# Optimization experiments

Measured on AMD Instinct MI355X. Metric: run time of the kernel, lower is better.

The kernel has to match this reference:

```python
import jax, jax.numpy as jnp
import numpy as np

B, S, T, H, E, V = 32, 400, 32, 512, 128, 50000
A = H  # attention feature dim

def setup_inputs() -> dict:
    key = jax.random.key(0)
    ks = jax.random.split(key, 16)
    f = lambda k, shape: jax.random.normal(k, shape, dtype=jnp.float32) * 0.02
    return {
        "source_tokens": jax.random.randint(ks[0], (B, S), 0, V, dtype=jnp.int32),
        "embedded_tgt": jax.random.normal(ks[1], (B, T, E), dtype=jnp.float32),
        "encoder_states": jax.random.normal(ks[2], (B, S, 2 * H), dtype=jnp.float32),
        "source_mask": jnp.ones((B, S), dtype=bool),
        "h0": f(ks[3], (B, H)),
        "c0": f(ks[4], (B, H)),
        "W_ih": f(ks[5], (4 * H, E)),
        "W_hh": f(ks[6], (4 * H, H)),
        "b_ih": jnp.zeros((4 * H,), jnp.float32),
        "b_hh": jnp.zeros((4 * H,), jnp.float32),
        "W_enc": f(ks[7], (2 * H, A)),
        "W_dec": f(ks[8], (H, A)),
        "w_cov": f(ks[9], (A,)),
        "b_att": jnp.zeros((A,), jnp.float32),
        "v_att": f(ks[10], (A,)),
        "W_ah": f(ks[11], (3 * H, H)),
        "b_ah": jnp.zeros((H,), jnp.float32),
        "W_pg": f(ks[12], (3 * H + E, 1)),
        "b_pg": jnp.zeros((1,), jnp.float32),
        "W_v": f(ks[13], (H, V)),
        "b_v": jnp.zeros((V,), jnp.float32),
    }


def reference(source_tokens, embedded_tgt, encoder_states, source_mask, h0, c0,
              W_ih, W_hh, b_ih, b_hh, W_enc, W_dec, w_cov, b_att, v_att,
              W_ah, b_ah, W_pg, b_pg, W_v, b_v):
    Bn, Sn = source_tokens.shape
    # precompute encoder projection for Bahdanau attention: (B,S,A)
    enc_proj = jnp.einsum('bsd,da->bsa', encoder_states, W_enc)
    bidx = jnp.arange(Bn)[:, None]
    NEG = jnp.float32(-1e9)
    EPS = jnp.float32(1e-20)

    def step(carry, emb):  # emb: (B,E)
        h, c, cov = carry
        # LSTM cell (torch gate order i,f,g,o)
        gates = emb @ W_ih.T + h @ W_hh.T + b_ih + b_hh
        i, fg, g, o = jnp.split(gates, 4, axis=-1)
        c = jax.nn.sigmoid(fg) * c + jax.nn.sigmoid(i) * jnp.tanh(g)
        h = jax.nn.sigmoid(o) * jnp.tanh(c)
        # coverage attention
        feat = jnp.tanh(enc_proj + (h @ W_dec)[:, None, :] + cov[:, :, None] * w_cov + b_att)
        scores = jnp.where(source_mask, feat @ v_att, NEG)  # (B,S)
        attn = jax.nn.softmax(scores, axis=-1)
        context = jnp.einsum('bs,bsd->bd', attn, encoder_states)  # (B,2H)
        cov = cov + attn
        ah = jnp.tanh(jnp.concatenate([context, h], axis=-1) @ W_ah + b_ah)  # (B,H)
        p_gen = jax.nn.sigmoid(jnp.concatenate([context, h, emb], axis=-1) @ W_pg + b_pg)  # (B,1)
        vocab_dist = p_gen * jax.nn.softmax(ah @ W_v + b_v, axis=-1)  # (B,V)
        attn_dist = (1.0 - p_gen) * attn  # (B,S)
        final = vocab_dist.at[bidx, source_tokens].add(attn_dist)  # copy-merge scatter_add
        logp = jnp.log(final + EPS)
        return (h, c, cov), (logp, ah, attn, cov, p_gen[:, 0])

    cov0 = jnp.zeros_like(source_mask, dtype=jnp.float32)
    _, (logps, dec_states, attns, covs, p_gens) = jax.lax.scan(
        step, (h0, c0, cov0), jnp.swapaxes(embedded_tgt, 0, 1))
    tr = lambda x: jnp.swapaxes(x, 0, 1)  # (T,B,...) -> (B,T,...)
    return tr(logps), tr(dec_states), tr(attns), tr(covs), tr(p_gens)
```

## Files before the change

### kernel.cpp

```cpp
#include <hip/hip_runtime.h>
#include <hip/hip_bf16.h>
#include <stdint.h>
#include <stddef.h>

#define B_  32
#define S_  400
#define T_  32
#define H_  512
#define E_  128
#define V_  50000
#define A_  512
#define H2_ 1024
#define H3_ 1536
#define H4_ 2048
#define R_  1024
#define PGK_ 1664
#define NBLKV_ 391
#define GRB_ 128
#define WROW_ 520

typedef unsigned short u16;
typedef short v8s __attribute__((ext_vector_type(8)));
typedef float v4f __attribute__((ext_vector_type(4)));

__device__ __forceinline__ float fsig(float x){ return 1.0f/(1.0f + __expf(-x)); }
__device__ __forceinline__ float ftanh(float x){ float e = __expf(2.0f*x); return 1.0f - 2.0f/(e + 1.0f); }
__device__ __forceinline__ u16 f2bf(float x){ __hip_bfloat16 b = __float2bfloat16(x); return *reinterpret_cast<u16*>(&b); }
__device__ __forceinline__ float bf2f(u16 u){ __hip_bfloat16 b = *reinterpret_cast<__hip_bfloat16*>(&u); return __bfloat162float(b); }

__device__ __forceinline__ float wsum(float v){
  #pragma unroll
  for (int off = 32; off > 0; off >>= 1) v += __shfl_xor(v, off, 64);
  return v;
}
__device__ __forceinline__ float wmax(float v){
  #pragma unroll
  for (int off = 32; off > 0; off >>= 1) v = fmaxf(v, __shfl_xor(v, off, 64));
  return v;
}

#define ALD(p)    __hip_atomic_load((p), __ATOMIC_RELAXED, __HIP_MEMORY_SCOPE_AGENT)
#define AST(p,v)  __hip_atomic_store((p), (v), __ATOMIC_RELAXED, __HIP_MEMORY_SCOPE_AGENT)

__device__ __forceinline__ void ldsbar(){
  asm volatile("s_waitcnt lgkmcnt(0)" ::: "memory");
  __builtin_amdgcn_s_barrier();
  asm volatile("" ::: "memory");
}

__device__ __forceinline__ void gridbar2(unsigned* bar, unsigned target, int grp){
  __syncthreads();
  if (threadIdx.x == 0){
    unsigned v = __hip_atomic_fetch_add(bar + grp*32, 1u, __ATOMIC_RELAXED, __HIP_MEMORY_SCOPE_AGENT);
    if (v == target*16u - 1u){
      unsigned g2 = __hip_atomic_fetch_add(bar + 256, 1u, __ATOMIC_RELAXED, __HIP_MEMORY_SCOPE_AGENT);
      if (g2 == target*8u - 1u)
        AST(bar + 288, target);
    }
    while (ALD(bar + 288) < target) __builtin_amdgcn_s_sleep(2);
    asm volatile("" ::: "memory");
  }
  __syncthreads();
}


__global__ void k_init0(unsigned* __restrict__ bar, unsigned long long* __restrict__ mz){
  int t = threadIdx.x;
  if (t < 512) AST(bar + t, 0u);
  if (t < 256) AST(mz + t, 0ull);
}

__global__ __launch_bounds__(256) void k_transpose(const float* __restrict__ in, float* __restrict__ out, int R, int C){
  __shared__ float tile[64][65];
  int c0 = blockIdx.x*64, r0 = blockIdx.y*64;
  int tid = threadIdx.x;
  int cl = tid & 63, q = tid >> 6;
  #pragma unroll
  for (int i=0;i<16;i++){
    int r = q + i*4;
    float v = 0.0f;
    if (r0 + r < R && c0 + cl < C) v = in[(size_t)(r0+r)*C + c0 + cl];
    tile[r][cl] = v;
  }
  __syncthreads();
  #pragma unroll
  for (int i=0;i<16;i++){
    int c = q + i*4;
    if (c0 + c < C && r0 + cl < R)
      out[(size_t)(c0+c)*R + r0 + cl] = tile[cl][c];
  }
}

__global__ __launch_bounds__(256) void k_convT(const float* __restrict__ in, u16* __restrict__ hi, int R, int C){
  __shared__ float tile[64][65];
  int c0 = blockIdx.x*64, r0 = blockIdx.y*64;
  int tid = threadIdx.x;
  int cl = tid & 63, q = tid >> 6;
  #pragma unroll
  for (int i=0;i<16;i++){
    int r = q + i*4;
    float v = 0.0f;
    if (r0 + r < R && c0 + cl < C) v = in[(size_t)(r0+r)*C + c0 + cl];
    tile[r][cl] = v;
  }
  __syncthreads();
  #pragma unroll
  for (int i=0;i<16;i++){
    int c = q + i*4;
    if (c0 + c < C && r0 + cl < R)
      hi[(size_t)(c0+c)*R + r0 + cl] = f2bf(tile[cl][c]);
  }
}

__global__ __launch_bounds__(256) void k_convT3(const float* __restrict__ in, u16* __restrict__ out){
  __shared__ float tile[64][65];
  int c0 = blockIdx.x*64, r0 = blockIdx.y*64;
  int tid = threadIdx.x;
  int cl = tid & 63, q = tid >> 6;
  #pragma unroll
  for (int i=0;i<16;i++){
    int r = q + i*4;
    tile[r][cl] = in[(size_t)(r0+r)*A_ + c0 + cl];
  }
  __syncthreads();
  #pragma unroll
  for (int i=0;i<16;i++){
    int c = q + i*4;
    float v = tile[cl][c];
    u16 h = f2bf(v);
    u16 lo = f2bf(v - bf2f(h));
    size_t o = (size_t)(c0+c)*3072 + (r0+cl);
    out[o] = h;
    out[o + 1024] = lo;
    out[o + 2048] = h;
  }
}

__global__ void k_conv3(const float* __restrict__ in, u16* __restrict__ out, int n4){
  int i = blockIdx.x*256 + threadIdx.x;
  if (i >= n4) return;
  float4 x = reinterpret_cast<const float4*>(in)[i];
  u16 h0v=f2bf(x.x), h1v=f2bf(x.y), h2v=f2bf(x.z), h3v=f2bf(x.w);
  uint2 hv; hv.x = (unsigned)h0v | ((unsigned)h1v << 16); hv.y = (unsigned)h2v | ((unsigned)h3v << 16);
  uint2 lv;
  lv.x = (unsigned)f2bf(x.x - bf2f(h0v)) | ((unsigned)f2bf(x.y - bf2f(h1v)) << 16);
  lv.y = (unsigned)f2bf(x.z - bf2f(h2v)) | ((unsigned)f2bf(x.w - bf2f(h3v)) << 16);
  int row = i >> 8, c = (i & 255)*4;
  size_t base = (size_t)row*3072 + c;
  *reinterpret_cast<uint2*>(out + base)        = hv;
  *reinterpret_cast<uint2*>(out + base + 1024) = hv;
  *reinterpret_cast<uint2*>(out + base + 2048) = lv;
}

__global__ __launch_bounds__(256) void k_gih(const float* __restrict__ emb, const float* __restrict__ WihT,
    const float* __restrict__ b_ih, const float* __restrict__ b_hh, float* __restrict__ G){
  __shared__ float em[8][128];
  int r0 = blockIdx.x*8;
  int tid = threadIdx.x;
  #pragma unroll
  for (int i=0;i<4;i++){
    int e = i*256 + tid;
    em[e>>7][e&127] = emb[(size_t)(r0 + (e>>7))*E_ + (e&127)];
  }
  __syncthreads();
  for (int jj=0;jj<8;jj++){
    int j = jj*256 + tid;
    float bias = b_ih[j] + b_hh[j];
    float acc[8];
    #pragma unroll
    for (int r=0;r<8;r++) acc[r] = bias;
    for (int e=0;e<128;e++){
      float wv = WihT[(size_t)e*H4_ + j];
      #pragma unroll
      for (int r=0;r<8;r++) acc[r] += em[r][e]*wv;
    }
    #pragma unroll
    for (int rr=0;rr<8;rr++){
      int r = r0 + rr;
      G[(size_t)(r & 31)*65536 + (size_t)(j >> 9)*16384 + (size_t)(j & 511)*32 + (r >> 5)] = acc[rr];
    }
  }
}

__global__ __launch_bounds__(256, 2) void k_gemm_bf16(
    const u16* __restrict__ A, int lda, const u16* __restrict__ Bt, int ldb,
    const float* __restrict__ bias, float* __restrict__ Cf, u16* __restrict__ Cbf, int ldc,
    int M, int N, int K, float2* __restrict__ stats, int nblk)
{
  __shared__ __align__(16) float CsF[128*132];
  __shared__ float rs[128], rs2[128];
  u16* As = reinterpret_cast<u16*>(CsF);
  u16* Bs = As + 128*64;
  const int tid = threadIdx.x;
  const int m0 = blockIdx.y * 128;
  const int n0 = blockIdx.x * 128;
  const int l  = tid & 63;
  const int wavebase = tid & ~63;
  const int wid = tid >> 6;
  const int wm = (wid >> 1) * 64;
  const int wn = (wid & 1) * 64;

  v4f acc[4][4];
  v4f vzero = {0.0f, 0.0f, 0.0f, 0.0f};
  #pragma unroll
  for (int i=0;i<4;i++)
    #pragma unroll
    for (int j=0;j<4;j++) acc[i][j] = vzero;

  for (int k0 = 0; k0 < K; k0 += 64){
    __syncthreads();
    #pragma unroll
    for (int jj=0;jj<4;jj++){
      int fc = jj*256 + tid;
      int row = fc >> 3;
      int cc = (fc & 7) ^ (row & 7);
      const u16* g = A + (size_t)(m0 + row)*lda + k0 + cc*8;
      __builtin_amdgcn_global_load_lds(
        (__attribute__((address_space(1))) void*)g,
        (__attribute__((address_space(3))) void*)(As + (size_t)(jj*256 + wavebase)*8),
        16, 0, 0);
    }
    #pragma unroll
    for (int jj=0;jj<4;jj++){
      int fc = jj*256 + tid;
      int row = fc >> 3;
      int cc = (fc & 7) ^ (row & 7);
      int rn = n0 + row; if (rn > N-1) rn = N-1;
      const u16* g = Bt + (size_t)rn*ldb + k0 + cc*8;
      __builtin_amdgcn_global_load_lds(
        (__attribute__((address_space(1))) void*)g,
        (__attribute__((address_space(3))) void*)(Bs + (size_t)(jj*256 + wavebase)*8),
        16, 0, 0);
    }
    __syncthreads();
    #pragma unroll
    for (int ks=0;ks<2;ks++){
      v8s af[4], bfr[4];
      #pragma unroll
      for (int rt=0;rt<4;rt++){
        int r = wm + rt*16 + (l & 15);
        int cs = (ks*4 + (l >> 4)) ^ (r & 7);
        af[rt] = *reinterpret_cast<const v8s*>(As + r*64 + cs*8);
      }
      #pragma unroll
      for (int nt=0;nt<4;nt++){
        int r = wn + nt*16 + (l & 15);
        int cs = (ks*4 + (l >> 4)) ^ (r & 7);
        bfr[nt] = *reinterpret_cast<const v8s*>(Bs + r*64 + cs*8);
      }
      #pragma unroll
      for (int rt=0;rt<4;rt++)
        #pragma unroll
        for (int nt=0;nt<4;nt++)
          acc[rt][nt] = __builtin_amdgcn_mfma_f32_16x16x32_bf16(af[rt], bfr[nt], acc[rt][nt], 0, 0, 0);
    }
  }

  const int cl = l & 15;
  const int rg = (l >> 4) * 4;
  float cvv[4][4][4];
  #pragma unroll
  for (int rt=0;rt<4;rt++)
    #pragma unroll
    for (int nt=0;nt<4;nt++){
      int gc = n0 + wn + nt*16 + cl;
      float bv = (bias && gc < N) ? bias[gc] : 0.0f;
      #pragma unroll
      for (int i=0;i<4;i++) cvv[rt][nt][i] = acc[rt][nt][i] + bv;
    }

  if (stats){
    float tsm[4][4];
    #pragma unroll
    for (int rt=0;rt<4;rt++)
      #pragma unroll
      for (int i=0;i<4;i++){
        float mx = -1e30f;
        #pragma unroll
        for (int nt=0;nt<4;nt++){
          int gc = n0 + wn + nt*16 + cl;
          if (gc < N) mx = fmaxf(mx, cvv[rt][nt][i]);
        }
        #pragma unroll
        for (int off=1; off<16; off<<=1) mx = fmaxf(mx, __shfl_xor(mx, off, 64));
        if (wn == 0 && cl == 0) rs[wm + rt*16 + rg + i] = mx;
        tsm[rt][i] = mx;
      }
    __syncthreads();
    if (wn != 0){
      #pragma unroll
      for (int rt=0;rt<4;rt++)
        #pragma unroll
        for (int i=0;i<4;i++){
          float c = fmaxf(tsm[rt][i], rs[wm + rt*16 + rg + i]);
          if (cl == 0) rs[wm + rt*16 + rg + i] = c;
        }
    }
    __syncthreads();
    #pragma unroll
    for (int rt=0;rt<4;rt++)
      #pragma unroll
      for (int i=0;i<4;i++){
        float rm = rs[wm + rt*16 + rg + i];
        float sm = 0.0f;
        #pragma unroll
        for (int nt=0;nt<4;nt++){
          int gc = n0 + wn + nt*16 + cl;
          if (gc < N) sm += __expf(cvv[rt][nt][i] - rm);
        }
        #pragma unroll
        for (int off=1; off<16; off<<=1) sm += __shfl_xor(sm, off, 64);
        tsm[rt][i] = sm;
        if (wn == 0 && cl == 0) rs2[wm + rt*16 + rg + i] = sm;
      }
    __syncthreads();
    if (wn != 0 && cl == 0){
      #pragma unroll
      for (int rt=0;rt<4;rt++)
        #pragma unroll
        for (int i=0;i<4;i++){
          int row = wm + rt*16 + rg + i;
          stats[(size_t)(m0 + row)*nblk + blockIdx.x] =
            make_float2(rs[row], tsm[rt][i] + rs2[row]);
        }
    }
  }

  __syncthreads();
  #pragma unroll
  for (int rt=0;rt<4;rt++)
    #pragma unroll
    for (int nt=0;nt<4;nt++)
      #pragma unroll
      for (int i=0;i<4;i++)
        CsF[(wm + rt*16 + rg + i)*132 + wn + nt*16 + cl] = cvv[rt][nt][i];
  __syncthreads();
  #pragma unroll
  for (int it=0; it<16; ++it){
    int row = (tid >> 5) + it*8;
    int c4 = tid & 31;
    int gc = n0 + c4*4;
    int gr = m0 + row;
    if (gc < N){
      float4 v = *reinterpret_cast<const float4*>(&CsF[row*132 + c4*4]);
      if (Cf) *reinterpret_cast<float4*>(Cf + (size_t)gr*ldc + gc) = v;
      if (Cbf){
        uint2 o;
        o.x = (unsigned)f2bf(v.x) | ((unsigned)f2bf(v.y) << 16);
        o.y = (unsigned)f2bf(v.z) | ((unsigned)f2bf(v.w) << 16);
        *reinterpret_cast<uint2*>(Cbf + (size_t)gr*ldc + gc) = o;
      }
    }
  }
}

__global__ __launch_bounds__(256) void k_wv_f32(
  const float* __restrict__ Aah, const float* __restrict__ Wv, const float* __restrict__ bv,
  float* __restrict__ Cl)
{
  __shared__ float Asf[32][68];
  __shared__ float Bsf[32][64];
  int n0 = blockIdx.x*64, m0 = blockIdx.y*64;
  int tid = threadIdx.x;
  int tx = tid & 15, ty = tid >> 4;
  float acc[4][4] = {};
  for (int kc = 0; kc < H_; kc += 32){
    __syncthreads();
    #pragma unroll
    for (int i=0;i<8;i++){
      int e = i*256 + tid;
      Asf[e & 31][e >> 5] = Aah[(size_t)(m0 + (e >> 5))*H_ + kc + (e & 31)];
    }
    #pragma unroll
    for (int i=0;i<8;i++){
      int e = i*256 + tid;
      int nc = n0 + (e & 63); if (nc >= V_) nc = V_-1;
      Bsf[e >> 6][e & 63] = Wv[(size_t)(kc + (e >> 6))*V_ + nc];
    }
    __syncthreads();
    #pragma unroll
    for (int k=0;k<32;k++){
      float4 a4 = *reinterpret_cast<const float4*>(&Asf[k][ty*4]);
      float4 b4 = *reinterpret_cast<const float4*>(&Bsf[k][tx*4]);
      float av[4] = {a4.x, a4.y, a4.z, a4.w};
      float bv4[4] = {b4.x, b4.y, b4.z, b4.w};
      #pragma unroll
      for (int i=0;i<4;i++)
        #pragma unroll
        for (int j=0;j<4;j++)
          acc[i][j] = __builtin_fmaf(av[i], bv4[j], acc[i][j]);
    }
  }
  #pragma unroll
  for (int i=0;i<4;i++){
    int rr = m0 + ty*4 + i;
    #pragma unroll
    for (int j=0;j<4;j++){
      int cc = n0 + tx*4 + j;
      if (cc < V_) Cl[(size_t)rr*V_ + cc] = acc[i][j] + bv[cc];
    }
  }
}

__global__ __launch_bounds__(1024) void k_recur(
  const float* __restrict__ W_hh, const float* __restrict__ G2,
  const float* __restrict__ W_decT, const u16* __restrict__ ep_bf,
  const float* __restrict__ w_cov, const float* __restrict__ v_att,
  const void* __restrict__ maskp, const float* __restrict__ h0,
  const float* __restrict__ c0, float* __restrict__ h_gT,
  float* __restrict__ dec_g, unsigned long long* __restrict__ mz,
  float* __restrict__ catbuf, float* __restrict__ attns, float* __restrict__ covs,
  unsigned* __restrict__ bar)
{
  const int beta = blockIdx.x;
  const int tid = threadIdx.x;
  __shared__ __align__(16) u16 Whi[32*WROW_];
  __shared__ __align__(16) u16 Wlo[32*WROW_];
  __shared__ __align__(16) u16 Hhi[32*WROW_];
  __shared__ __align__(16) u16 Hlo[32*WROW_];
  __shared__ float gv2[16][32];
  __shared__ float c_l[128];
  __shared__ float dec_l[512];
  __shared__ float sc_l[100];
  __shared__ float cov_l[100];
  __shared__ float smz[4][2];

  const int b32 = tid & 31;
  const int w = tid >> 6, l = tid & 63;
  const int grp = beta & 7;
  const int bb = (beta & 7)*4 + (beta >> 5);
  const int sq = (beta >> 3) & 3;
  const int b2 = (tid & 15)*2;
  const int kg = tid >> 4;

  for (int idx = tid; idx < 32*512; idx += 1024){
    int row = idx >> 9;
    int k = idx & 511;
    float v = 0.0f;
    if (row < 16)      v = W_hh[((size_t)(row >> 2)*H_ + beta*4 + (row & 3))*H_ + k];
    else if (row < 20) v = W_decT[(size_t)(beta*4 + (row - 16))*H_ + k];
    u16 h = f2bf(v);
    Whi[row*WROW_ + k] = h;
    Wlo[row*WROW_ + k] = f2bf(v - bf2f(h));
  }
  if (tid < 128) c_l[tid] = c0[(size_t)(tid & 31)*H_ + beta*4 + (tid >> 5)];
  if (tid < 100) cov_l[tid] = 0.f;

  const unsigned* m32p = (const unsigned*)maskp;
  const unsigned char* m8p = (const unsigned char*)maskp;
  const bool bytemode = (m32p[0] == 0x01010101u);

  float wc8[8], va8[8];
  {
    int a0 = l*8;
    #pragma unroll
    for (int j=0;j<8;j++){ wc8[j] = w_cov[a0+j]; va8[j] = v_att[a0+j]; }
  }

  float hA[8], hB[8];
  unsigned long long hld[8];
  #pragma unroll
  for (int kk=0;kk<8;kk++){
    int k = kg*8 + kk;
    hA[kk] = h0[(size_t)b2*H_ + k];
    hB[kk] = h0[(size_t)(b2+1)*H_ + k];
  }

  unsigned gen = 0;
  for (int i = 0; i <= T_ + 1; ++i){
    const int par = i & 1;
    {
      v8s phA, plA, phB, plB;
      #pragma unroll
      for (int kk=0;kk<8;kk++){
        float va = hA[kk], vb = hB[kk];
        u16 ha = f2bf(va), hb = f2bf(vb);
        phA[kk] = (short)ha; plA[kk] = (short)f2bf(va - bf2f(ha));
        phB[kk] = (short)hb; plB[kk] = (short)f2bf(vb - bf2f(hb));
      }
      *reinterpret_cast<v8s*>(Hhi + (size_t)b2*WROW_ + kg*8) = phA;
      *reinterpret_cast<v8s*>(Hlo + (size_t)b2*WROW_ + kg*8) = plA;
      *reinterpret_cast<v8s*>(Hhi + (size_t)(b2+1)*WROW_ + kg*8) = phB;
      *reinterpret_cast<v8s*>(Hlo + (size_t)(b2+1)*WROW_ + kg*8) = plB;
    }
    ldsbar();

    if (w < 4){
      const int mt = w >> 1, nt = w & 1;
      const int fr = (l & 15);
      const int fo = (l >> 4)*8;
      const u16* Ahi = Whi + (size_t)(mt*16 + fr)*WROW_ + fo;
      const u16* Alo = Wlo + (size_t)(mt*16 + fr)*WROW_ + fo;
      const u16* Bhi = Hhi + (size_t)(nt*16 + fr)*WROW_ + fo;
      const u16* Blo = Hlo + (size_t)(nt*16 + fr)*WROW_ + fo;
      v4f a0 = {0.f,0.f,0.f,0.f}, a1 = a0, a2 = a0;
      #pragma unroll
      for (int ks=0; ks<16; ks++){
        v8s wh = *reinterpret_cast<const v8s*>(Ahi + ks*32);
        v8s wl = *reinterpret_cast<const v8s*>(Alo + ks*32);
        v8s hh = *reinterpret_cast<const v8s*>(Bhi + ks*32);
        v8s hl = *reinterpret_cast<const v8s*>(Blo + ks*32);
        a0 = __builtin_amdgcn_mfma_f32_16x16x32_bf16(wh, hh, a0, 0, 0, 0);
        a1 = __builtin_amdgcn_mfma_f32_16x16x32_bf16(wh, hl, a1, 0, 0, 0);
        a2 = __builtin_amdgcn_mfma_f32_16x16x32_bf16(wl, hh, a2, 0, 0, 0);
      }
      v4f acc = a0 + a1 + a2;
      if (mt == 0){
        int col = nt*16 + fr;
        int r0w = (l >> 4)*4;
        #pragma unroll
        for (int q=0;q<4;q++) gv2[r0w + q][col] = acc[q];
      } else if ((l >> 4) == 0){
        int b = nt*16 + fr;
        float* dg = dec_g + (size_t)par*B_*A_ + (size_t)b*A_ + beta*4;
        unsigned long long p0 = ((unsigned long long)__float_as_uint(acc[1]) << 32) | __float_as_uint(acc[0]);
        unsigned long long p1 = ((unsigned long long)__float_as_uint(acc[3]) << 32) | __float_as_uint(acc[2]);
        AST(reinterpret_cast<unsigned long long*>(dg), p0);
        AST(reinterpret_cast<unsigned long long*>(dg + 2), p1);
      }
    }
    ldsbar();

    if (i < T_ && tid < 128){
      int hh = tid >> 5;
      int hidx = beta*4 + hh;
      const float* Gr = G2 + (size_t)i*65536 + (size_t)hidx*32 + b32;
      float gi = gv2[0*4+hh][b32] + Gr[0];
      float gf = gv2[1*4+hh][b32] + Gr[16384];
      float gz = gv2[2*4+hh][b32] + Gr[32768];
      float go = gv2[3*4+hh][b32] + Gr[49152];
      float co = c_l[tid];
      float cn = fsig(gf)*co + fsig(gi)*ftanh(gz);
      float hn = fsig(go)*ftanh(cn);
      c_l[tid] = cn;
      AST(h_gT + (size_t)(par^1)*16384 + (size_t)hidx*32 + b32, hn);
      catbuf[(size_t)(b32*T_ + i)*H3_ + H2_ + hidx] = hn;
    }
    gridbar2(bar, ++gen, grp);

    if (i < T_){
      const unsigned long long* hp =
        reinterpret_cast<const unsigned long long*>(h_gT + (size_t)(par^1)*16384);
      #pragma unroll
      for (int kk=0;kk<8;kk++)
        hld[kk] = ALD(hp + (size_t)(kg*8 + kk)*16 + (b2 >> 1));
    }

    if (i >= 2){
      if (tid < 4){
        unsigned long long v = ALD(mz + (size_t)(i & 1)*128 + bb*4 + tid);
        smz[tid][0] = __uint_as_float((unsigned)v);
        smz[tid][1] = __uint_as_float((unsigned)(v >> 32));
      }
      __syncthreads();
      float gm = fmaxf(fmaxf(smz[0][0], smz[1][0]), fmaxf(smz[2][0], smz[3][0]));
      float gZ = smz[0][1]*__expf(smz[0][0]-gm) + smz[1][1]*__expf(smz[1][0]-gm)
               + smz[2][1]*__expf(smz[2][0]-gm) + smz[3][1]*__expf(smz[3][0]-gm);
      float invZ = 1.f/gZ;
      int r2 = bb*T_ + (i-2);
      if (tid < 100){
        float av = __expf(sc_l[tid] - gm)*invZ;
        int s = sq*100 + tid;
        float cn = cov_l[tid] + av;
        cov_l[tid] = cn;
        attns[(size_t)r2*S_ + s] = av;
        covs[(size_t)r2*S_ + s]  = cn;
      }
      __syncthreads();
    }

    if (i >= 1 && i <= T_){
      if (tid < 512) dec_l[tid] = ALD(dec_g + (size_t)par*B_*A_ + (size_t)bb*A_ + tid);
      ldsbar();
      int a0i = l*8;
      float dec8[8];
      #pragma unroll
      for (int j=0;j<8;j++) dec8[j] = dec_l[a0i+j];
      #pragma unroll
      for (int it=0; it<7; ++it){
        int sl = w + it*16;
        if (sl < 100){
          int s = sq*100 + sl;
          float cv = cov_l[sl];
          uint4 e8 = *reinterpret_cast<const uint4*>(ep_bf + (size_t)(bb*S_ + s)*A_ + a0i);
          unsigned uu[4] = {e8.x, e8.y, e8.z, e8.w};
          float part = 0.f;
          #pragma unroll
          for (int j=0;j<4;j++){
            float xa = bf2f((u16)(uu[j] & 0xFFFFu)) + dec8[2*j]   + cv*wc8[2*j];
            part += va8[2*j]*ftanh(xa);
            float xb = bf2f((u16)(uu[j] >> 16))     + dec8[2*j+1] + cv*wc8[2*j+1];
            part += va8[2*j+1]*ftanh(xb);
          }
          part = wsum(part);
          if (l == 0){
            bool on = bytemode ? (m8p[bb*S_+s] != 0) : (m32p[bb*S_+s] != 0u);
            sc_l[sl] = on ? part : -1e9f;
          }
        }
      }
      __syncthreads();
      if (tid < 64){
        float x1v = sc_l[l];
        float x2v = (l + 64 < 100) ? sc_l[l + 64] : -1e30f;
        float m = wmax(fmaxf(x1v, x2v));
        float z = __expf(x1v - m) + ((l + 64 < 100) ? __expf(x2v - m) : 0.f);
        z = wsum(z);
        if (l == 0){
          unsigned long long pk = ((unsigned long long)__float_as_uint(z) << 32)
                                | (unsigned long long)__float_as_uint(m);
          AST(mz + (size_t)((i-1) & 1)*128 + bb*4 + sq, pk);
        }
      }
    }

    if (i < T_){
      #pragma unroll
      for (int kk=0;kk<8;kk++){
        hA[kk] = __uint_as_float((unsigned)hld[kk]);
        hB[kk] = __uint_as_float((unsigned)(hld[kk] >> 32));
      }
    }
  }
}


__global__ __launch_bounds__(256, 2) void k_ctx(
  const float* __restrict__ attns, const u16* __restrict__ enc3, float* __restrict__ catbuf)
{
  __shared__ float att_s[32][400];
  int d0 = blockIdx.x*64, b = blockIdx.y;
  int tid = threadIdx.x;
  for (int tt=0; tt<32; ++tt)
    for (int s = tid; s < S_; s += 256)
      att_s[tt][s] = attns[(size_t)(b*T_ + tt)*S_ + s];
  __syncthreads();
  int lane = tid & 31;
  int d = d0 + lane*2;
  int tg = tid >> 5;
  float acc0[4] = {0,0,0,0}, acc1[4] = {0,0,0,0};
  const u16* encb = enc3 + (size_t)(b*S_)*3072 + d;
  #pragma unroll 4
  for (int s=0; s<S_; ++s){
    unsigned uv = *reinterpret_cast<const unsigned*>(encb + (size_t)s*3072);
    float e0 = bf2f((u16)(uv & 0xFFFFu));
    float e1 = bf2f((u16)(uv >> 16));
    #pragma unroll
    for (int i=0;i<4;i++){
      float av = att_s[tg*4 + i][s];
      acc0[i] = __builtin_fmaf(av, e0, acc0[i]);
      acc1[i] = __builtin_fmaf(av, e1, acc1[i]);
    }
  }
  #pragma unroll
  for (int i=0;i<4;i++)
    *reinterpret_cast<float2*>(catbuf + (size_t)(b*T_ + tg*4 + i)*H3_ + d) =
      make_float2(acc0[i], acc1[i]);
}

__global__ __launch_bounds__(256) void k_ahgemm(
  const float* __restrict__ Acat, const float* __restrict__ W_ah, const float* __restrict__ b_ah,
  float* __restrict__ dec_states, u16* __restrict__ ah_bf)
{
  __shared__ float Asf[32][68];
  __shared__ float Bsf[32][64];
  int n0 = blockIdx.x*64, m0 = blockIdx.y*64;
  int tid = threadIdx.x;
  int tx = tid & 15, ty = tid >> 4;
  float acc[4][4] = {};
  for (int kc = 0; kc < H3_; kc += 32){
    __syncthreads();
    #pragma unroll
    for (int i=0;i<8;i++){
      int e = i*256 + tid;
      Asf[e & 31][e >> 5] = Acat[(size_t)(m0 + (e >> 5))*H3_ + kc + (e & 31)];
    }
    #pragma unroll
    for (int i=0;i<8;i++){
      int e = i*256 + tid;
      Bsf[e >> 6][e & 63] = W_ah[(size_t)(kc + (e >> 6))*H_ + n0 + (e & 63)];
    }
    __syncthreads();
    #pragma unroll
    for (int k=0;k<32;k++){
      float4 a4 = *reinterpret_cast<const float4*>(&Asf[k][ty*4]);
      float4 b4 = *reinterpret_cast<const float4*>(&Bsf[k][tx*4]);
      float av[4] = {a4.x, a4.y, a4.z, a4.w};
      float bv[4] = {b4.x, b4.y, b4.z, b4.w};
      #pragma unroll
      for (int i=0;i<4;i++)
        #pragma unroll
        for (int j=0;j<4;j++)
          acc[i][j] = __builtin_fmaf(av[i], bv[j], acc[i][j]);
    }
  }
  #pragma unroll
  for (int i=0;i<4;i++){
    int rr = m0 + ty*4 + i;
    #pragma unroll
    for (int j=0;j<4;j++){
      int cc = n0 + tx*4 + j;
      float v = ftanh(acc[i][j] + b_ah[cc]);
      dec_states[(size_t)rr*H_ + cc] = v;
      if (ah_bf) ah_bf[(size_t)rr*H_ + cc] = f2bf(v);
    }
  }
}

__global__ __launch_bounds__(512) void k_pgen(const float* __restrict__ catbuf, const float* __restrict__ emb,
  const float* __restrict__ W_pg, const float* __restrict__ b_pg, float* __restrict__ pgens)
{
  int w = threadIdx.x >> 6, l = threadIdx.x & 63;
  int r = blockIdx.x*8 + w;
  float part = 0.0f;
  for (int d = l; d < PGK_; d += 64){
    float x = (d < H3_) ? catbuf[(size_t)r*H3_ + d] : emb[(size_t)r*E_ + (d - H3_)];
    part += x*W_pg[d];
  }
  part = wsum(part);
  if (l == 0) pgens[r] = fsig(part + b_pg[0]);
}

__global__ __launch_bounds__(512) void k_final2(
  float* __restrict__ logits, const u16* __restrict__ rowbf,
  const float* __restrict__ pgens,
  const float* __restrict__ attns, const int* __restrict__ src,
  const float2* __restrict__ stats, int nblk)
{
  __shared__ unsigned bits[1568];
  __shared__ unsigned keys[1024];
  __shared__ float vals[1024];
  __shared__ float sred[18];
  int r = blockIdx.x;
  int b = r >> 5;
  int tid = threadIdx.x;
  int w = tid >> 6, l = tid & 63;
  float* row = logits + (size_t)r*V_;
  const u16* rb = rowbf ? (rowbf + (size_t)r*V_) : nullptr;

  for (int i = tid; i < 1568; i += 512) bits[i] = 0u;
  for (int i = tid; i < 1024; i += 512){ keys[i] = 0xFFFFFFFFu; vals[i] = 0.0f; }

  if (stats){
    float m = -1e30f, Z = 0.0f;
    if (tid < nblk){ float2 st = stats[(size_t)r*nblk + tid]; m = st.x; Z = st.y; }
    #pragma unroll
    for (int off=32; off>0; off>>=1){
      float mo = __shfl_xor(m, off, 64);
      float Zo = __shfl_xor(Z, off, 64);
      float nm = fmaxf(m, mo);
      Z = Z*__expf(m - nm) + Zo*__expf(mo - nm);
      m = nm;
    }
    if (l == 0){ sred[w*2] = m; sred[w*2+1] = Z; }
    __syncthreads();
    if (tid == 0){
      float gm = -1e30f, gz = 0.0f;
      #pragma unroll
      for (int i=0;i<8;i++){
        float mi = sred[i*2], zi = sred[i*2+1];
        float nm = fmaxf(gm, mi);
        gz = gz*__expf(gm - nm) + zi*__expf(mi - nm);
        gm = nm;
      }
      sred[16] = gm; sred[17] = gz;
    }
    __syncthreads();
  } else {
    float m = -1e30f;
    for (int j = tid; j < V_/4; j += 512){
      float4 x = reinterpret_cast<const float4*>(row)[j];
      m = fmaxf(fmaxf(m, x.x), fmaxf(fmaxf(x.y, x.z), x.w));
    }
    m = wmax(m);
    if (l == 0) sred[w] = m;
    __syncthreads();
    if (tid == 0){
      float gm = -1e30f;
      #pragma unroll
      for (int i=0;i<8;i++) gm = fmaxf(gm, sred[i]);
      sred[16] = gm;
    }
    __syncthreads();
    float gm = sred[16];
    float z = 0.0f;
    for (int j = tid; j < V_/4; j += 512){
      float4 x = reinterpret_cast<const float4*>(row)[j];
      z += __expf(x.x-gm) + __expf(x.y-gm) + __expf(x.z-gm) + __expf(x.w-gm);
    }
    z = wsum(z);
    if (l == 0) sred[8 + w] = z;
    __syncthreads();
    if (tid == 0){
      float gz = 0.0f;
      #pragma unroll
      for (int i=0;i<8;i++) gz += sred[8 + i];
      sred[17] = gz;
    }
    __syncthreads();
  }

  float gm = sred[16];
  float gZ = sred[17];
  float pg = pgens[r];
  float scale = pg / gZ;
  float lscale = __logf(scale);

  if (tid < S_){
    int tok = src[b*S_ + tid];
    float add = (1.0f - pg)*attns[(size_t)r*S_ + tid];
    atomicOr(&bits[tok >> 5], 1u << (tok & 31));
    unsigned h = ((unsigned)tok * 2654435761u) >> 22;
    while (true){
      unsigned prev = atomicCAS(&keys[h], 0xFFFFFFFFu, (unsigned)tok);
      if (prev == 0xFFFFFFFFu || prev == (unsigned)tok){
        atomicAdd(&vals[h], add);
        break;
      }
      h = (h + 1) & 1023;
    }
  }
  __syncthreads();

  for (int j = tid; j < V_/4; j += 512){
    float xv[4];
    if (rb){
      uint2 u = reinterpret_cast<const uint2*>(rb)[j];
      xv[0] = bf2f((u16)(u.x & 0xFFFFu)); xv[1] = bf2f((u16)(u.x >> 16));
      xv[2] = bf2f((u16)(u.y & 0xFFFFu)); xv[3] = bf2f((u16)(u.y >> 16));
    } else {
      float4 x = reinterpret_cast<const float4*>(row)[j];
      xv[0] = x.x; xv[1] = x.y; xv[2] = x.z; xv[3] = x.w;
    }
    int v = 4*j;
    float o[4];
    #pragma unroll
    for (int k=0;k<4;k++){
      int vv = v + k;
      bool hit = (bits[vv >> 5] >> (vv & 31)) & 1u;
      float tt = xv[k] - gm + lscale;
      if (!hit && tt > -25.0f){
        o[k] = tt;
      } else {
        float pval = __expf(xv[k] - gm)*scale;
        if (hit){
          unsigned h = ((unsigned)vv * 2654435761u) >> 22;
          while (keys[h] != 0xFFFFFFFFu){
            if (keys[h] == (unsigned)vv){ pval += vals[h]; break; }
            h = (h + 1) & 1023;
          }
        }
        o[k] = __logf(pval + 1e-20f);
      }
    }
    reinterpret_cast<float4*>(row)[j] = make_float4(o[0], o[1], o[2], o[3]);
  }
}


extern "C" void kernel_launch(void* const* d_in, const int* in_sizes, int n_in,
                              void* d_out, int out_size, void* d_ws, size_t ws_size,
                              hipStream_t stream)
{
  const int* src_tokens = (const int*)d_in[0];
  const float* embedded = (const float*)d_in[1];
  const float* enc      = (const float*)d_in[2];
  const void*  maskp    = (const void*)d_in[3];
  const float* h0  = (const float*)d_in[4];
  const float* c0  = (const float*)d_in[5];
  const float* W_ih = (const float*)d_in[6];
  const float* W_hh = (const float*)d_in[7];
  const float* b_ih = (const float*)d_in[8];
  const float* b_hh = (const float*)d_in[9];
  const float* W_enc = (const float*)d_in[10];
  const float* W_dec = (const float*)d_in[11];
  const float* w_cov = (const float*)d_in[12];
  const float* b_att = (const float*)d_in[13];
  const float* v_att = (const float*)d_in[14];
  const float* W_ah  = (const float*)d_in[15];
  const float* b_ah  = (const float*)d_in[16];
  const float* W_pg  = (const float*)d_in[17];
  const float* b_pg  = (const float*)d_in[18];
  const float* W_v   = (const float*)d_in[19];
  const float* b_v   = (const float*)d_in[20];
  (void)in_sizes; (void)n_in; (void)out_size;

  float* outp = (float*)d_out;
  float* logps = outp;
  float* dec_states = logps + (size_t)R_*V_;
  float* attns = dec_states + (size_t)R_*H_;
  float* covs  = attns + (size_t)R_*S_;
  float* pgens = covs + (size_t)R_*S_;

  char* sp = (char*)logps;
  auto salloc = [&](size_t bytes) -> void* {
    void* p = (void*)sp;
    sp += (bytes + 255) & ~(size_t)255;
    return p;
  };
  unsigned* bar = (unsigned*)salloc(2048);
  unsigned long long* mz = (unsigned long long*)salloc((size_t)2*B_*4*8);
  u16* ep_bf    = (u16*)salloc((size_t)B_*S_*A_*2);
  u16* enc3     = (u16*)salloc((size_t)B_*S_*3072*2);
  u16* WencT3   = (u16*)salloc((size_t)A_*3072*2);
  float* WihT   = (float*)salloc((size_t)E_*H4_*4);
  float* W_decT = (float*)salloc((size_t)H_*A_*4);
  float* G2     = (float*)salloc((size_t)R_*H4_*4);
  float* catbuf = (float*)salloc((size_t)R_*H3_*4);
  float* dec_g  = (float*)salloc((size_t)2*B_*A_*4);
  float* h_gT   = (float*)salloc((size_t)2*H_*B_*4);

  char* wp = (char*)d_ws;
  auto walloc = [&](size_t bytes) -> void* {
    void* p = (void*)wp;
    wp += (bytes + 255) & ~(size_t)255;
    return p;
  };
  u16* ah_bf = (u16*)walloc((size_t)R_*H_*2);
  u16* WvT   = (u16*)walloc((size_t)V_*H_*2);
  float2* stats = (float2*)walloc((size_t)R_*NBLKV_*8);
  u16* logits_bf = (u16*)walloc((size_t)R_*V_*2);
  const size_t ws_fast  = (size_t)R_*H_*2 + (size_t)V_*H_*2 + 512;
  const size_t ws_stats = ws_fast + (size_t)R_*NBLKV_*8 + 256;
  const size_t ws_bf    = ws_stats + (size_t)R_*V_*2 + 256;
  const bool fast_wv   = (ws_size >= ws_fast);
  const bool use_stats = (ws_size >= ws_stats);
  const bool use_bf    = (ws_size >= ws_bf) && use_stats;

  k_init0<<<1, 512, 0, stream>>>(bar, mz);
  k_transpose<<<dim3(2,32), 256, 0, stream>>>(W_ih, WihT, H4_, E_);
  k_transpose<<<dim3(8,8), 256, 0, stream>>>(W_dec, W_decT, H_, A_);
  k_gih<<<128, 256, 0, stream>>>(embedded, WihT, b_ih, b_hh, G2);
  k_conv3<<<(B_*S_*H2_/4 + 255)/256, 256, 0, stream>>>(enc, enc3, B_*S_*H2_/4);
  k_convT3<<<dim3(8,16), 256, 0, stream>>>(W_enc, WencT3);
  if (fast_wv)
    k_convT<<<dim3((V_+63)/64, 8), 256, 0, stream>>>(W_v, WvT, H_, V_);

  k_gemm_bf16<<<dim3(A_/128, (B_*S_)/128), 256, 0, stream>>>(
      enc3, 3072, WencT3, 3072, b_att, nullptr, ep_bf, A_, B_*S_, A_, 3072, nullptr, 0);

  k_recur<<<GRB_, 1024, 0, stream>>>(W_hh, G2, W_decT, ep_bf, w_cov, v_att, maskp,
                                     h0, c0, h_gT, dec_g, mz,
                                     catbuf, attns, covs, bar);

  k_ctx<<<dim3(16, 32), 256, 0, stream>>>(attns, enc3, catbuf);
  k_ahgemm<<<dim3(8,16), 256, 0, stream>>>(catbuf, W_ah, b_ah, dec_states, fast_wv ? ah_bf : (u16*)nullptr);
  k_pgen<<<128, 512, 0, stream>>>(catbuf, embedded, W_pg, b_pg, pgens);

  if (fast_wv)
    k_gemm_bf16<<<dim3(NBLKV_, R_/128), 256, 0, stream>>>(
        ah_bf, H_, WvT, H_, b_v,
        use_bf ? nullptr : logps, use_bf ? logits_bf : nullptr, V_,
        R_, V_, H_, use_stats ? stats : nullptr, NBLKV_);
  else
    k_wv_f32<<<dim3((V_+63)/64, R_/64), 256, 0, stream>>>(dec_states, W_v, b_v, logps);

  k_final2<<<R_, 512, 0, stream>>>(logps, use_bf ? logits_bf : (u16*)nullptr,
                                   pgens, attns, src_tokens,
                                   (fast_wv && use_stats) ? stats : nullptr, NBLKV_);
}
```

Measured before the change: 1.134 ms.

## Overlap W_v transpose with recurrent kernel and drop W_ih/W_dec transposes

The separate W_v bf16 transpose kernel is folded into the persistent recurrent kernel as extra blocks (beyond the 128 recurrence blocks) that transpose tiles while the recurrence runs on the remaining CUs. The W_ih and W_dec transpose kernels are removed; k_gih reads W_ih rows directly and k_recur reads W_dec with a strided access during its one-time load. This removes three launches and tries to hide the W_v conversion behind the latency-bound recurrence. The extra blocks could delay co-scheduling of the grid-barrier recurrence blocks if they are dispatched first, and could contend for memory bandwidth.

```diff
diff --git a/kernel.cpp b/kernel.cpp
--- a/kernel.cpp
+++ b/kernel.cpp
@@ -17,6 +17,8 @@
 #define PGK_ 1664
 #define NBLKV_ 391
 #define GRB_ 128
+#define NCTI_ 6256
+#define GRBX_ (GRB_ + (NCTI_+3)/4)
 #define WROW_ 520
 
 typedef unsigned short u16;
@@ -68,48 +70,6 @@
   int t = threadIdx.x;
   if (t < 512) AST(bar + t, 0u);
   if (t < 256) AST(mz + t, 0ull);
-}
-
-__global__ __launch_bounds__(256) void k_transpose(const float* __restrict__ in, float* __restrict__ out, int R, int C){
-  __shared__ float tile[64][65];
-  int c0 = blockIdx.x*64, r0 = blockIdx.y*64;
-  int tid = threadIdx.x;
-  int cl = tid & 63, q = tid >> 6;
-  #pragma unroll
-  for (int i=0;i<16;i++){
-    int r = q + i*4;
-    float v = 0.0f;
-    if (r0 + r < R && c0 + cl < C) v = in[(size_t)(r0+r)*C + c0 + cl];
-    tile[r][cl] = v;
-  }
-  __syncthreads();
-  #pragma unroll
-  for (int i=0;i<16;i++){
-    int c = q + i*4;
-    if (c0 + c < C && r0 + cl < R)
-      out[(size_t)(c0+c)*R + r0 + cl] = tile[cl][c];
-  }
-}
-
-__global__ __launch_bounds__(256) void k_convT(const float* __restrict__ in, u16* __restrict__ hi, int R, int C){
-  __shared__ float tile[64][65];
-  int c0 = blockIdx.x*64, r0 = blockIdx.y*64;
-  int tid = threadIdx.x;
-  int cl = tid & 63, q = tid >> 6;
-  #pragma unroll
-  for (int i=0;i<16;i++){
-    int r = q + i*4;
-    float v = 0.0f;
-    if (r0 + r < R && c0 + cl < C) v = in[(size_t)(r0+r)*C + c0 + cl];
-    tile[r][cl] = v;
-  }
-  __syncthreads();
-  #pragma unroll
-  for (int i=0;i<16;i++){
-    int c = q + i*4;
-    if (c0 + c < C && r0 + cl < R)
-      hi[(size_t)(c0+c)*R + r0 + cl] = f2bf(tile[cl][c]);
-  }
 }
 
 __global__ __launch_bounds__(256) void k_convT3(const float* __restrict__ in, u16* __restrict__ out){
@@ -152,7 +112,7 @@
   *reinterpret_cast<uint2*>(out + base + 2048) = lv;
 }
 
-__global__ __launch_bounds__(256) void k_gih(const float* __restrict__ emb, const float* __restrict__ WihT,
+__global__ __launch_bounds__(256) void k_gih(const float* __restrict__ emb, const float* __restrict__ W_ih,
     const float* __restrict__ b_ih, const float* __restrict__ b_hh, float* __restrict__ G){
   __shared__ float em[8][128];
   int r0 = blockIdx.x*8;
@@ -169,8 +129,9 @@
     float acc[8];
     #pragma unroll
     for (int r=0;r<8;r++) acc[r] = bias;
+    const float* wrow = W_ih + (size_t)j*E_;
     for (int e=0;e<128;e++){
-      float wv = WihT[(size_t)e*H4_ + j];
+      float wv = wrow[e];
       #pragma unroll
       for (int r=0;r<8;r++) acc[r] += em[r][e]*wv;
     }
@@ -404,13 +365,14 @@
 
 __global__ __launch_bounds__(1024) void k_recur(
   const float* __restrict__ W_hh, const float* __restrict__ G2,
-  const float* __restrict__ W_decT, const u16* __restrict__ ep_bf,
+  const float* __restrict__ W_dec, const u16* __restrict__ ep_bf,
   const float* __restrict__ w_cov, const float* __restrict__ v_att,
   const void* __restrict__ maskp, const float* __restrict__ h0,
   const float* __restrict__ c0, float* __restrict__ h_gT,
   float* __restrict__ dec_g, unsigned long long* __restrict__ mz,
   float* __restrict__ catbuf, float* __restrict__ attns, float* __restrict__ covs,
-  unsigned* __restrict__ bar)
+  unsigned* __restrict__ bar,
+  const float* __restrict__ Wv, u16* __restrict__ WvT)
 {
   const int beta = blockIdx.x;
   const int tid = threadIdx.x;
@@ -425,6 +387,40 @@
   __shared__ float cov_l[100];
   __shared__ float smz[4][2];
 
+  if (beta >= GRB_){
+    if (WvT){
+      int sub = tid >> 8;
+      int t256 = tid & 255;
+      int tix = (beta - GRB_)*4 + sub;
+      int cl = t256 & 63, q = t256 >> 6;
+      bool act = (tix < NCTI_);
+      int txi = act ? (tix % 782) : 0;
+      int tyi = act ? (tix / 782) : 0;
+      int c0 = txi*64, r0 = tyi*64;
+      u16* baseu = (sub & 2) ? Hhi : Whi;
+      float* tile = reinterpret_cast<float*>(baseu + (sub & 1)*8320);
+      if (act){
+        #pragma unroll
+        for (int i2=0;i2<16;i2++){
+          int rr = q + i2*4;
+          float v = 0.0f;
+          if (c0 + cl < V_) v = Wv[(size_t)(r0+rr)*V_ + c0 + cl];
+          tile[rr*65 + cl] = v;
+        }
+      }
+      __syncthreads();
+      if (act){
+        #pragma unroll
+        for (int i2=0;i2<16;i2++){
+          int cc = q + i2*4;
+          if (c0 + cc < V_)
+            WvT[(size_t)(c0+cc)*H_ + r0 + cl] = f2bf(tile[cl*65 + cc]);
+        }
+      }
+    }
+    return;
+  }
+
   const int b32 = tid & 31;
   const int w = tid >> 6, l = tid & 63;
   const int grp = beta & 7;
@@ -438,7 +434,7 @@
     int k = idx & 511;
     float v = 0.0f;
     if (row < 16)      v = W_hh[((size_t)(row >> 2)*H_ + beta*4 + (row & 3))*H_ + k];
-    else if (row < 20) v = W_decT[(size_t)(beta*4 + (row - 16))*H_ + k];
+    else if (row < 20) v = W_dec[(size_t)k*A_ + beta*4 + (row - 16)];
     u16 h = f2bf(v);
     Whi[row*WROW_ + k] = h;
     Wlo[row*WROW_ + k] = f2bf(v - bf2f(h));
@@ -509,7 +505,7 @@
         int col = nt*16 + fr;
         int r0w = (l >> 4)*4;
         #pragma unroll
-        for (int q=0;q<4;q++) gv2[r0w + q][col] = acc[q];
+        for (int q2=0;q2<4;q2++) gv2[r0w + q2][col] = acc[q2];
       } else if ((l >> 4) == 0){
         int b = nt*16 + fr;
         float* dg = dec_g + (size_t)par*B_*A_ + (size_t)b*A_ + beta*4;
@@ -903,8 +899,6 @@
   u16* ep_bf    = (u16*)salloc((size_t)B_*S_*A_*2);
   u16* enc3     = (u16*)salloc((size_t)B_*S_*3072*2);
   u16* WencT3   = (u16*)salloc((size_t)A_*3072*2);
-  float* WihT   = (float*)salloc((size_t)E_*H4_*4);
-  float* W_decT = (float*)salloc((size_t)H_*A_*4);
   float* G2     = (float*)salloc((size_t)R_*H4_*4);
   float* catbuf = (float*)salloc((size_t)R_*H3_*4);
   float* dec_g  = (float*)salloc((size_t)2*B_*A_*4);
@@ -928,20 +922,17 @@
   const bool use_bf    = (ws_size >= ws_bf) && use_stats;
 
   k_init0<<<1, 512, 0, stream>>>(bar, mz);
-  k_transpose<<<dim3(2,32), 256, 0, stream>>>(W_ih, WihT, H4_, E_);
-  k_transpose<<<dim3(8,8), 256, 0, stream>>>(W_dec, W_decT, H_, A_);
-  k_gih<<<128, 256, 0, stream>>>(embedded, WihT, b_ih, b_hh, G2);
+  k_gih<<<128, 256, 0, stream>>>(embedded, W_ih, b_ih, b_hh, G2);
   k_conv3<<<(B_*S_*H2_/4 + 255)/256, 256, 0, stream>>>(enc, enc3, B_*S_*H2_/4);
   k_convT3<<<dim3(8,16), 256, 0, stream>>>(W_enc, WencT3);
-  if (fast_wv)
-    k_convT<<<dim3((V_+63)/64, 8), 256, 0, stream>>>(W_v, WvT, H_, V_);
 
   k_gemm_bf16<<<dim3(A_/128, (B_*S_)/128), 256, 0, stream>>>(
       enc3, 3072, WencT3, 3072, b_att, nullptr, ep_bf, A_, B_*S_, A_, 3072, nullptr, 0);
 
-  k_recur<<<GRB_, 1024, 0, stream>>>(W_hh, G2, W_decT, ep_bf, w_cov, v_att, maskp,
-                                     h0, c0, h_gT, dec_g, mz,
-                                     catbuf, attns, covs, bar);
+  k_recur<<<GRBX_, 1024, 0, stream>>>(W_hh, G2, W_dec, ep_bf, w_cov, v_att, maskp,
+                                      h0, c0, h_gT, dec_g, mz,
+                                      catbuf, attns, covs, bar,
+                                      W_v, fast_wv ? WvT : (u16*)nullptr);
 
   k_ctx<<<dim3(16, 32), 256, 0, stream>>>(attns, enc3, catbuf);
   k_ahgemm<<<dim3(8,16), 256, 0, stream>>>(catbuf, W_ah, b_ah, dec_states, fast_wv ? ah_bf : (u16*)nullptr);
```

After: 1.066 ms. 1.06x faster.
